# Optimization experiments

Measured on AMD Instinct MI355X. Metric: run time of the kernel, lower is better.

The kernel has to match this reference:

```python
import jax, jax.numpy as jnp
import numpy as np

NEG_SLOPE = 0.2   # PyG GATConv default negative_slope
BN_EPS = 1e-5
N_NODES = 50000
N_EDGES = 600000
N_GRAPHS = 64


def _gat_conv(x, W, att_src, att_dst, bias, src, dst, heads, out_ch, concat):
    """PyG GATConv (eval mode, self-loops already appended to src/dst).
    x: [N, in], W: [in, heads*out_ch], att_*: [heads, out_ch], bias: [heads*out_ch] or [out_ch].
    """
    n = x.shape[0]
    h = (x @ W).reshape(n, heads, out_ch)                  # [N, H, C]
    a_s = jnp.sum(h * att_src[None], axis=-1)              # [N, H]
    a_d = jnp.sum(h * att_dst[None], axis=-1)              # [N, H]
    logit = jax.nn.leaky_relu(a_s[src] + a_d[dst], NEG_SLOPE)  # [E, H]
    # segment softmax over destination node (every node has a self-loop -> no empty segment)
    m = jax.ops.segment_max(logit, dst, num_segments=n)
    p = jnp.exp(logit - m[dst])
    denom = jax.ops.segment_sum(p, dst, num_segments=n)
    alpha = p / (denom[dst] + 1e-16)                       # [E, H]
    out = jax.ops.segment_sum(h[src] * alpha[:, :, None], dst, num_segments=n)  # [N, H, C]
    out = out.reshape(n, heads * out_ch) if concat else out.mean(axis=1)
    return out + bias


def _bn(x, gamma, beta):
    mu = x.mean(axis=0)
    var = x.var(axis=0)
    return (x - mu) * jax.lax.rsqrt(var + BN_EPS) * gamma + beta


def setup_inputs() -> dict:
    key = jax.random.key(0)
    ks = jax.random.split(key, 20)
    hidden = 64
    d1_in, d1_out, h1 = 5, hidden // 2, 4          # 5 -> 32x4 = 128
    d2_in, d2_out, h2 = hidden * 2, hidden // 2, 4  # 128 -> 32x4 = 128
    d3_in, d3_out, h3 = hidden * 2, hidden, 1       # 128 -> 64

    def glorot(k, shape):
        fan = shape[0] + shape[-1]
        return jax.random.normal(k, shape, dtype=jnp.float32) * np.sqrt(2.0 / fan)

    inp = {
        "x": jax.random.normal(ks[0], (N_NODES, d1_in), dtype=jnp.float32),
        "edge_index": jax.random.randint(ks[1], (2, N_EDGES), 0, N_NODES),
        "batch": jnp.sort(jax.random.randint(ks[2], (N_NODES,), 0, N_GRAPHS)),
        # conv1
        "W1": glorot(ks[3], (d1_in, h1 * d1_out)),
        "a1_src": glorot(ks[4], (h1, d1_out)),
        "a1_dst": glorot(ks[5], (h1, d1_out)),
        "b1": jnp.zeros((h1 * d1_out,), dtype=jnp.float32),
        "g1": jnp.ones((h1 * d1_out,), dtype=jnp.float32),
        "be1": jnp.zeros((h1 * d1_out,), dtype=jnp.float32),
        # conv2
        "W2": glorot(ks[6], (d2_in, h2 * d2_out)),
        "a2_src": glorot(ks[7], (h2, d2_out)),
        "a2_dst": glorot(ks[8], (h2, d2_out)),
        "b2": jnp.zeros((h2 * d2_out,), dtype=jnp.float32),
        "g2": jnp.ones((h2 * d2_out,), dtype=jnp.float32),
        "be2": jnp.zeros((h2 * d2_out,), dtype=jnp.float32),
        # conv3 (single head, concat=False)
        "W3": glorot(ks[9], (d3_in, h3 * d3_out)),
        "a3_src": glorot(ks[10], (h3, d3_out)),
        "a3_dst": glorot(ks[11], (h3, d3_out)),
        "b3": jnp.zeros((d3_out,), dtype=jnp.float32),
    }
    return inp


def reference(x, edge_index, batch, W1, a1_src, a1_dst, b1, g1, be1,
              W2, a2_src, a2_dst, b2, g2, be2, W3, a3_src, a3_dst, b3):
    n = x.shape[0]
    loops = jnp.arange(n)
    src = jnp.concatenate([edge_index[0], loops])  # PyG add_self_loops=True
    dst = jnp.concatenate([edge_index[1], loops])

    h = jax.nn.elu(_bn(_gat_conv(x, W1, a1_src, a1_dst, b1, src, dst, 4, 32, True), g1, be1))
    h = jax.nn.elu(_bn(_gat_conv(h, W2, a2_src, a2_dst, b2, src, dst, 4, 32, True), g2, be2))
    h = jax.nn.elu(_gat_conv(h, W3, a3_src, a3_dst, b3, src, dst, 1, 64, False))

    counts = jax.ops.segment_sum(jnp.ones((n,), h.dtype), batch, num_segments=N_GRAPHS)
    mean_pool = jax.ops.segment_sum(h, batch, num_segments=N_GRAPHS) / jnp.maximum(counts, 1.0)[:, None]
    max_pool = jax.ops.segment_max(h, batch, num_segments=N_GRAPHS)
    max_pool = jnp.where(counts[:, None] > 0, max_pool, 0.0)
    return jnp.concatenate([mean_pool, max_pool], axis=1)  # [G, 128]
```

## Files before the change

### kernel.cpp

```cpp
#include <hip/hip_runtime.h>
#include <math.h>

#define NEG_SLOPE 0.2f
#define BN_EPS 1e-5f

typedef __attribute__((ext_vector_type(8))) short short8;
typedef __attribute__((ext_vector_type(4))) float f32x4;

__device__ __forceinline__ float lrelu_f(float x){ return x > 0.f ? x : NEG_SLOPE * x; }
__device__ __forceinline__ float elu_f(float x){ return x > 0.f ? x : __expf(x) - 1.f; }

__device__ __forceinline__ unsigned short f2bf(float f){
    unsigned u = __float_as_uint(f);
    return (unsigned short)((u + 0x7fffu + ((u >> 16) & 1u)) >> 16);
}
__device__ __forceinline__ float bf_lo(unsigned v){ return __uint_as_float(v << 16); }
__device__ __forceinline__ float bf_hi(unsigned v){ return __uint_as_float(v & 0xffff0000u); }
__device__ __forceinline__ float bf2f(unsigned short b){ return __uint_as_float((unsigned)b << 16); }

__device__ __forceinline__ unsigned enc_f(float x){
    unsigned b = __float_as_uint(x);
    return (b & 0x80000000u) ? ~b : (b | 0x80000000u);
}
__device__ __forceinline__ float dec_f(unsigned u){
    return __uint_as_float((u & 0x80000000u) ? (u & 0x7FFFFFFFu) : ~u);
}

__global__ void k_prep(const int* __restrict__ ei, int E0, int N, int Bc, int Bg,
                       const int* __restrict__ batch, int G,
                       int* __restrict__ counts, int* __restrict__ gp,
                       const float* __restrict__ W1, const float* __restrict__ a1s,
                       const float* __restrict__ a1d,
                       const float* __restrict__ W2, const float* __restrict__ W3,
                       unsigned short* __restrict__ wt2, unsigned short* __restrict__ wt3,
                       float* __restrict__ u_s, float* __restrict__ u_d){
    int b = blockIdx.x, tid = threadIdx.x;
    if (b < Bc){
        int i = b * 256 + tid, tot = E0 + N;
        if (i < tot){
            int dst = (i < E0) ? ei[E0 + i] : (i - E0);
            atomicAdd(&counts[dst], 1);
        }
    } else if (b < Bc + Bg){
        int i = (b - Bc) * 256 + tid;
        if (i < N){
            int bb = batch[i];
            if (i == 0){ for (int g = 0; g <= bb; ++g) gp[g] = 0; }
            else { int pb = batch[i - 1]; for (int g = pb + 1; g <= bb; ++g) gp[g] = i; }
            if (i == N - 1){ for (int g = bb + 1; g <= G; ++g) gp[g] = N; }
        }
    } else if (b < Bc + Bg + 96){
        int i = (b - Bc - Bg) * 256 + tid;
        if (i < 128 * 128){
            int k = i / 128, c = i % 128;
            wt2[c * 128 + k] = f2bf(W2[i]);
        } else if (i < 128 * 128 + 128 * 64){
            int j = i - 128 * 128;
            int k = j / 64, c = j % 64;
            wt3[c * 128 + k] = f2bf(W3[j]);
        }
    } else {
        if (tid < 40){
            int t2 = tid % 20;
            int k = t2 / 4, hh = t2 % 4;
            const float* att = (tid < 20) ? a1s : a1d;
            float s = 0.f;
            for (int j = 0; j < 32; ++j) s += W1[k * 128 + hh * 32 + j] * att[hh * 32 + j];
            if (tid < 20) u_s[k * 4 + hh] = s; else u_d[k * 4 + hh] = s;
        }
    }
}

__global__ void k_scan_part(const int* __restrict__ counts, int n, int* __restrict__ part){
    __shared__ int sh[256];
    int tid = threadIdx.x;
    int i = blockIdx.x * 256 + tid;
    int v = (i < n) ? counts[i] : 0;
    sh[tid] = v;
    __syncthreads();
    for (int o = 128; o > 0; o >>= 1){
        if (tid < o) sh[tid] += sh[tid + o];
        __syncthreads();
    }
    if (tid == 0) part[blockIdx.x] = sh[0];
}

__global__ void k_scan_write(const int* __restrict__ counts, const int* __restrict__ part,
                             int n, int* __restrict__ row_ptr){
    __shared__ int sh[256], rsh[256];
    __shared__ int offs;
    int tid = threadIdx.x, bid = blockIdx.x;
    int po = 0;
    for (int j = tid; j < bid; j += 256) po += part[j];
    rsh[tid] = po;
    __syncthreads();
    for (int o = 128; o > 0; o >>= 1){
        if (tid < o) rsh[tid] += rsh[tid + o];
        __syncthreads();
    }
    if (tid == 0) offs = rsh[0];
    __syncthreads();
    int i = bid * 256 + tid;
    int v = (i < n) ? counts[i] : 0;
    sh[tid] = v;
    __syncthreads();
    for (int o = 1; o < 256; o <<= 1){
        int t = (tid >= o) ? sh[tid - o] : 0;
        __syncthreads();
        sh[tid] += t;
        __syncthreads();
    }
    if (i < n) row_ptr[i] = offs + sh[tid] - v;
    if (bid == gridDim.x - 1 && tid == 255) row_ptr[n] = offs + sh[255];
}

__global__ void k_scatter(const int* __restrict__ ei, int E0, int N,
                          const int* __restrict__ row_ptr, int* __restrict__ cursor,
                          int* __restrict__ csr_src){
    int i = blockIdx.x * blockDim.x + threadIdx.x;
    int tot = E0 + N;
    if (i >= tot) return;
    int src, dst;
    if (i < E0){ src = ei[i]; dst = ei[E0 + i]; } else { src = dst = i - E0; }
    int pos = atomicAdd(&cursor[dst], 1);
    csr_src[row_ptr[dst] + pos] = src;
}

__launch_bounds__(256)
__global__ void k_l1(const float* __restrict__ X, const float* __restrict__ W1,
                     const float* __restrict__ u_s, const float* __restrict__ u_d,
                     const int* __restrict__ row_ptr, const int* __restrict__ csr_src,
                     const float* __restrict__ bias, unsigned short* __restrict__ out, int N){
    __shared__ float Wl[5 * 128];
    int tid = threadIdx.x;
    for (int i = tid; i < 5 * 128; i += 256) Wl[i] = W1[i];
    __syncthreads();
    int grp = tid >> 4, ln = tid & 15;
    int hh = ln >> 2, sl = ln & 3;
    long n = (long)blockIdx.x * 16 + grp;
    if (n >= N) return;
    float us[5], ud[5];
#pragma unroll
    for (int k = 0; k < 5; ++k){ us[k] = u_s[k * 4 + hh]; ud[k] = u_d[k * 4 + hh]; }
    float ad = 0.f;
#pragma unroll
    for (int k = 0; k < 5; ++k) ad += X[n * 5 + k] * ud[k];
    int beg = row_ptr[n], end = row_ptr[n + 1];
    float y0 = 0.f, y1 = 0.f, y2 = 0.f, y3 = 0.f, y4 = 0.f, dn = 0.f;
    for (int e = beg + sl; e < end; e += 4){
        long s = csr_src[e];
        float x0 = X[s * 5 + 0], x1 = X[s * 5 + 1], x2 = X[s * 5 + 2],
              x3 = X[s * 5 + 3], x4 = X[s * 5 + 4];
        float as = x0 * us[0] + x1 * us[1] + x2 * us[2] + x3 * us[3] + x4 * us[4];
        float p = __expf(lrelu_f(as + ad));
        dn += p;
        y0 += p * x0; y1 += p * x1; y2 += p * x2; y3 += p * x3; y4 += p * x4;
    }
#pragma unroll
    for (int m = 1; m < 4; m <<= 1){
        y0 += __shfl_xor(y0, m); y1 += __shfl_xor(y1, m); y2 += __shfl_xor(y2, m);
        y3 += __shfl_xor(y3, m); y4 += __shfl_xor(y4, m); dn += __shfl_xor(dn, m);
    }
    float inv = 1.f / dn;
    y0 *= inv; y1 *= inv; y2 *= inv; y3 *= inv; y4 *= inv;
    int c0 = ln * 8;
    const float4* Wl4 = (const float4*)Wl;
    float4 oa, ob;
    {
        float4 w0a = Wl4[0 * 32 + ln * 2], w0b = Wl4[0 * 32 + ln * 2 + 1];
        float4 w1a = Wl4[1 * 32 + ln * 2], w1b = Wl4[1 * 32 + ln * 2 + 1];
        float4 w2a = Wl4[2 * 32 + ln * 2], w2b = Wl4[2 * 32 + ln * 2 + 1];
        float4 w3a = Wl4[3 * 32 + ln * 2], w3b = Wl4[3 * 32 + ln * 2 + 1];
        float4 w4a = Wl4[4 * 32 + ln * 2], w4b = Wl4[4 * 32 + ln * 2 + 1];
        oa.x = y0*w0a.x + y1*w1a.x + y2*w2a.x + y3*w3a.x + y4*w4a.x + bias[c0 + 0];
        oa.y = y0*w0a.y + y1*w1a.y + y2*w2a.y + y3*w3a.y + y4*w4a.y + bias[c0 + 1];
        oa.z = y0*w0a.z + y1*w1a.z + y2*w2a.z + y3*w3a.z + y4*w4a.z + bias[c0 + 2];
        oa.w = y0*w0a.w + y1*w1a.w + y2*w2a.w + y3*w3a.w + y4*w4a.w + bias[c0 + 3];
        ob.x = y0*w0b.x + y1*w1b.x + y2*w2b.x + y3*w3b.x + y4*w4b.x + bias[c0 + 4];
        ob.y = y0*w0b.y + y1*w1b.y + y2*w2b.y + y3*w3b.y + y4*w4b.y + bias[c0 + 5];
        ob.z = y0*w0b.z + y1*w1b.z + y2*w2b.z + y3*w3b.z + y4*w4b.z + bias[c0 + 6];
        ob.w = y0*w0b.w + y1*w1b.w + y2*w2b.w + y3*w3b.w + y4*w4b.w + bias[c0 + 7];
    }
    uint4 o;
    o.x = (unsigned)f2bf(oa.x) | ((unsigned)f2bf(oa.y) << 16);
    o.y = (unsigned)f2bf(oa.z) | ((unsigned)f2bf(oa.w) << 16);
    o.z = (unsigned)f2bf(ob.x) | ((unsigned)f2bf(ob.y) << 16);
    o.w = (unsigned)f2bf(ob.z) | ((unsigned)f2bf(ob.w) << 16);
    *(uint4*)&out[n * 128 + c0] = o;
}

template<int OUT, int H, bool BN>
__launch_bounds__(256)
__global__ void k_gemm_mfma(const unsigned short* __restrict__ X, const unsigned short* __restrict__ Wt,
                            const float* __restrict__ atts, const float* __restrict__ attd,
                            const float* __restrict__ coefs, const float* __restrict__ coefb,
                            unsigned short* __restrict__ h, float* __restrict__ as_,
                            float* __restrict__ ad_, int N){
    constexpr int TM  = 64;
    constexpr int NCT = OUT / 16;
    constexpr int CPH = NCT / H;
    __shared__ unsigned short Xl[TM * 128];
    __shared__ unsigned short Wl[OUT * 128];
    int tid = threadIdx.x;
    long base = (long)blockIdx.x * TM;

    for (int i = tid; i < OUT * 16; i += 256){
        int r = i >> 4, g = i & 15;
        uint4 v = *(const uint4*)&Wt[r * 128 + g * 8];
        int gs = g ^ (r & 7);
        *(uint4*)&Wl[r * 128 + gs * 8] = v;
    }
    for (int i = tid; i < TM * 16; i += 256){
        int r = i >> 4, g = i & 15;
        long node = base + r;
        uint4 o;
        if (node < N){
            uint4 raw = *(const uint4*)&X[node * 128 + g * 8];
            float f[8];
            f[0] = bf_lo(raw.x); f[1] = bf_hi(raw.x);
            f[2] = bf_lo(raw.y); f[3] = bf_hi(raw.y);
            f[4] = bf_lo(raw.z); f[5] = bf_hi(raw.z);
            f[6] = bf_lo(raw.w); f[7] = bf_hi(raw.w);
#pragma unroll
            for (int j = 0; j < 8; ++j){
                float v = f[j];
                if (BN) v = elu_f(fmaf(v, coefs[g * 8 + j], coefb[g * 8 + j]));
                f[j] = v;
            }
            o.x = (unsigned)f2bf(f[0]) | ((unsigned)f2bf(f[1]) << 16);
            o.y = (unsigned)f2bf(f[2]) | ((unsigned)f2bf(f[3]) << 16);
            o.z = (unsigned)f2bf(f[4]) | ((unsigned)f2bf(f[5]) << 16);
            o.w = (unsigned)f2bf(f[6]) | ((unsigned)f2bf(f[7]) << 16);
        } else {
            o.x = o.y = o.z = o.w = 0u;
        }
        int gs = g ^ (r & 7);
        *(uint4*)&Xl[r * 128 + gs * 8] = o;
    }
    __syncthreads();

    int wid = tid >> 6;
    int lane = tid & 63;
    int lr = lane & 15, lk = lane >> 4;

    short8 afrag[4];
    int arow = wid * 16 + lr;
#pragma unroll
    for (int ks = 0; ks < 4; ++ks){
        int g = ks * 4 + lk;
        int gs = g ^ (arow & 7);
        afrag[ks] = *(const short8*)&Xl[arow * 128 + gs * 8];
    }
    f32x4 acc[NCT];
#pragma unroll
    for (int ct = 0; ct < NCT; ++ct) acc[ct] = (f32x4){0.f, 0.f, 0.f, 0.f};
#pragma unroll
    for (int ct = 0; ct < NCT; ++ct){
        int brow = ct * 16 + lr;
#pragma unroll
        for (int ks = 0; ks < 4; ++ks){
            int g = ks * 4 + lk;
            int gs = g ^ (brow & 7);
            short8 bfrag = *(const short8*)&Wl[brow * 128 + gs * 8];
            acc[ct] = __builtin_amdgcn_mfma_f32_16x16x32_bf16(afrag[ks], bfrag, acc[ct], 0, 0, 0);
        }
    }
    float ps[H][4], pd[H][4];
#pragma unroll
    for (int hh = 0; hh < H; ++hh)
#pragma unroll
        for (int j = 0; j < 4; ++j){ ps[hh][j] = 0.f; pd[hh][j] = 0.f; }
#pragma unroll
    for (int ct = 0; ct < NCT; ++ct){
        int col = ct * 16 + lr;
        int hh = ct / CPH;
        float asv = atts[col], adv = attd[col];
#pragma unroll
        for (int j = 0; j < 4; ++j){
            float v = acc[ct][j];
            long node = base + wid * 16 + lk * 4 + j;
            if (node < N) h[node * OUT + col] = f2bf(v);
            ps[hh][j] += v * asv;
            pd[hh][j] += v * adv;
        }
    }
#pragma unroll
    for (int m = 1; m < 16; m <<= 1){
#pragma unroll
        for (int hh = 0; hh < H; ++hh)
#pragma unroll
            for (int j = 0; j < 4; ++j){
                ps[hh][j] += __shfl_xor(ps[hh][j], m);
                pd[hh][j] += __shfl_xor(pd[hh][j], m);
            }
    }
    if (lr == 0){
#pragma unroll
        for (int j = 0; j < 4; ++j){
            long node = base + wid * 16 + lk * 4 + j;
            if (node < N){
#pragma unroll
                for (int hh = 0; hh < H; ++hh){
                    as_[node * H + hh] = ps[hh][j];
                    ad_[node * H + hh] = pd[hh][j];
                }
            }
        }
    }
}

template<int C, int H, int ACT>
__global__ void k_agg(const unsigned short* __restrict__ h, const float* __restrict__ as_,
                      const float* __restrict__ ad_, const int* __restrict__ row_ptr,
                      const int* __restrict__ csr_src, const float* __restrict__ bias,
                      unsigned short* __restrict__ out, int N){
    constexpr int CPL = C / 64;
    constexpr int GROUP = C / H;
    int n = blockIdx.x;
    if (n >= N) return;
    int lane = threadIdx.x;
    int hh = (CPL * lane) / GROUP;
    float ad = ad_[n * H + hh];
    int beg = row_ptr[n], end = row_ptr[n + 1];
    float accx = 0.f, accy = 0.f, dn = 0.f;
    const unsigned* h32 = (const unsigned*)h;
    int e = beg;
    for (; e + 2 <= end; e += 2){
        int s0 = csr_src[e], s1 = csr_src[e + 1];
        float a0 = as_[s0 * H + hh], a1 = as_[s1 * H + hh];
        unsigned v0, v1; unsigned short w0, w1;
        if (CPL == 2){ v0 = h32[(long)s0 * 64 + lane]; v1 = h32[(long)s1 * 64 + lane]; }
        else { w0 = h[(long)s0 * 64 + lane]; w1 = h[(long)s1 * 64 + lane]; }
        float p0 = __expf(lrelu_f(a0 + ad));
        float p1 = __expf(lrelu_f(a1 + ad));
        dn += p0 + p1;
        if (CPL == 2){
            accx += p0 * bf_lo(v0) + p1 * bf_lo(v1);
            accy += p0 * bf_hi(v0) + p1 * bf_hi(v1);
        } else {
            accx += p0 * bf2f(w0) + p1 * bf2f(w1);
        }
    }
    if (e < end){
        int s0 = csr_src[e];
        float p0 = __expf(lrelu_f(as_[s0 * H + hh] + ad));
        dn += p0;
        if (CPL == 2){
            unsigned v0 = h32[(long)s0 * 64 + lane];
            accx += p0 * bf_lo(v0); accy += p0 * bf_hi(v0);
        } else {
            accx += p0 * bf2f(h[(long)s0 * 64 + lane]);
        }
    }
    float inv = 1.f / dn;
    if (CPL == 2){
        float vx = accx * inv + bias[2 * lane];
        float vy = accy * inv + bias[2 * lane + 1];
        if (ACT == 1){ vx = elu_f(vx); vy = elu_f(vy); }
        ((unsigned*)out)[(long)n * 64 + lane] =
            (unsigned)f2bf(vx) | ((unsigned)f2bf(vy) << 16);
    } else {
        float v = accx * inv + bias[lane];
        if (ACT == 1) v = elu_f(v);
        out[(long)n * 64 + lane] = f2bf(v);
    }
}

__launch_bounds__(256)
__global__ void k_bn_part(const unsigned short* __restrict__ x, int N,
                          float* __restrict__ ps, float* __restrict__ pq){
    __shared__ float ls[256 * 8], lq[256 * 8];
    int tid = threadIdx.x;
    int cg = tid & 15;
    int rg = tid >> 4;
    int rpb = (N + gridDim.x - 1) / gridDim.x;
    int lo = blockIdx.x * rpb;
    int hi = lo + rpb; if (hi > N) hi = N;
    float s[8], q[8];
#pragma unroll
    for (int j = 0; j < 8; ++j){ s[j] = 0.f; q[j] = 0.f; }
    int r = lo + rg;
    for (; r + 16 < hi; r += 32){
        uint4 va = *(const uint4*)&x[(long)r * 128 + cg * 8];
        uint4 vb = *(const uint4*)&x[(long)(r + 16) * 128 + cg * 8];
        float fa[8], fb[8];
        fa[0]=bf_lo(va.x); fa[1]=bf_hi(va.x); fa[2]=bf_lo(va.y); fa[3]=bf_hi(va.y);
        fa[4]=bf_lo(va.z); fa[5]=bf_hi(va.z); fa[6]=bf_lo(va.w); fa[7]=bf_hi(va.w);
        fb[0]=bf_lo(vb.x); fb[1]=bf_hi(vb.x); fb[2]=bf_lo(vb.y); fb[3]=bf_hi(vb.y);
        fb[4]=bf_lo(vb.z); fb[5]=bf_hi(vb.z); fb[6]=bf_lo(vb.w); fb[7]=bf_hi(vb.w);
#pragma unroll
        for (int j = 0; j < 8; ++j){
            s[j] += fa[j] + fb[j];
            q[j] += fa[j] * fa[j] + fb[j] * fb[j];
        }
    }
    for (; r < hi; r += 16){
        uint4 va = *(const uint4*)&x[(long)r * 128 + cg * 8];
        float fa[8];
        fa[0]=bf_lo(va.x); fa[1]=bf_hi(va.x); fa[2]=bf_lo(va.y); fa[3]=bf_hi(va.y);
        fa[4]=bf_lo(va.z); fa[5]=bf_hi(va.z); fa[6]=bf_lo(va.w); fa[7]=bf_hi(va.w);
#pragma unroll
        for (int j = 0; j < 8; ++j){ s[j] += fa[j]; q[j] += fa[j] * fa[j]; }
    }
#pragma unroll
    for (int j = 0; j < 8; ++j){ ls[tid * 8 + j] = s[j]; lq[tid * 8 + j] = q[j]; }
    __syncthreads();
    for (int o = 8; o > 0; o >>= 1){
        if (rg < o){
#pragma unroll
            for (int j = 0; j < 8; ++j){
                s[j] += ls[(tid + o * 16) * 8 + j];
                q[j] += lq[(tid + o * 16) * 8 + j];
                ls[tid * 8 + j] = s[j]; lq[tid * 8 + j] = q[j];
            }
        }
        __syncthreads();
    }
    if (rg == 0){
#pragma unroll
        for (int j = 0; j < 8; ++j){
            ps[(long)blockIdx.x * 128 + cg * 8 + j] = s[j];
            pq[(long)blockIdx.x * 128 + cg * 8 + j] = q[j];
        }
    }
}

__launch_bounds__(1024)
__global__ void k_bn_fin(const float* __restrict__ ps, const float* __restrict__ pq, int PB,
                         const float* __restrict__ g, const float* __restrict__ be,
                         float invN, float* __restrict__ cs, float* __restrict__ cb){
    __shared__ float sh_s[1024], sh_q[1024];
    int tid = threadIdx.x;
    int c = tid & 127, sl = tid >> 7;
    float s = 0.f, q = 0.f;
    for (int b = sl; b < PB; b += 8){
        s += ps[(long)b * 128 + c];
        q += pq[(long)b * 128 + c];
    }
    sh_s[tid] = s; sh_q[tid] = q;
    __syncthreads();
    for (int o = 4; o > 0; o >>= 1){
        if (sl < o){
            s += sh_s[tid + o * 128]; q += sh_q[tid + o * 128];
            sh_s[tid] = s; sh_q[tid] = q;
        }
        __syncthreads();
    }
    if (sl == 0){
        float mu = s * invN;
        float var = q * invN - mu * mu;
        float sc = g[c] * rsqrtf(var + BN_EPS);
        cs[c] = sc;
        cb[c] = be[c] - mu * sc;
    }
}

__global__ void k_pool_part(const unsigned short* __restrict__ x, const int* __restrict__ gp,
                            float* __restrict__ psum, unsigned* __restrict__ pmax){
    constexpr int S = 16;
    __shared__ float2 ssum[256], smax[256];
    int g = blockIdx.y;
    int split = blockIdx.x;
    int tid = threadIdx.x;
    int c2 = tid & 31, sub = tid >> 5;
    int beg = gp[g], end = gp[g + 1];
    int len = end - beg;
    int chunk = (len + S - 1) / S;
    int lo = beg + split * chunk;
    int hi = lo + chunk; if (hi > end) hi = end;
    if (lo >= hi) return;
    float sx = 0.f, sy = 0.f, mx = -1e30f, my = -1e30f;
    const unsigned* xr = (const unsigned*)x;
    for (int i = lo + sub; i < hi; i += 8){
        unsigned v = xr[(long)i * 32 + c2];
        float a = bf_lo(v), b = bf_hi(v);
        sx += a; sy += b;
        mx = fmaxf(mx, a); my = fmaxf(my, b);
    }
    ssum[tid] = make_float2(sx, sy); smax[tid] = make_float2(mx, my);
    __syncthreads();
    for (int o = 4; o > 0; o >>= 1){
        if (sub < o){
            float2 s2 = ssum[tid + o * 32], m2 = smax[tid + o * 32];
            sx += s2.x; sy += s2.y;
            mx = fmaxf(mx, m2.x); my = fmaxf(my, m2.y);
            ssum[tid] = make_float2(sx, sy); smax[tid] = make_float2(mx, my);
        }
        __syncthreads();
    }
    if (sub == 0){
        atomicAdd(&psum[g * 64 + c2 * 2], sx);
        atomicAdd(&psum[g * 64 + c2 * 2 + 1], sy);
        atomicMax(&pmax[g * 64 + c2 * 2], enc_f(mx));
        atomicMax(&pmax[g * 64 + c2 * 2 + 1], enc_f(my));
    }
}

__global__ void k_pool_fin(const float* __restrict__ psum, const unsigned* __restrict__ pmax,
                           const int* __restrict__ gp, float* __restrict__ out){
    int g = blockIdx.x;
    int c = threadIdx.x;
    int cnt = gp[g + 1] - gp[g];
    float mean = (cnt > 0) ? psum[g * 64 + c] / (float)cnt : 0.f;
    float mx   = (cnt > 0) ? dec_f(pmax[g * 64 + c]) : 0.f;
    out[g * 128 + c]      = mean;
    out[g * 128 + 64 + c] = mx;
}

extern "C" void kernel_launch(void* const* d_in, const int* in_sizes, int n_in,
                              void* d_out, int out_size, void* d_ws, size_t ws_size,
                              hipStream_t stream){
    const float* x   = (const float*)d_in[0];
    const int*   ei  = (const int*)d_in[1];
    const int*   bat = (const int*)d_in[2];
    const float* W1  = (const float*)d_in[3];
    const float* a1s = (const float*)d_in[4];
    const float* a1d = (const float*)d_in[5];
    const float* b1  = (const float*)d_in[6];
    const float* g1  = (const float*)d_in[7];
    const float* be1 = (const float*)d_in[8];
    const float* W2  = (const float*)d_in[9];
    const float* a2s = (const float*)d_in[10];
    const float* a2d = (const float*)d_in[11];
    const float* b2  = (const float*)d_in[12];
    const float* g2  = (const float*)d_in[13];
    const float* be2 = (const float*)d_in[14];
    const float* W3  = (const float*)d_in[15];
    const float* a3s = (const float*)d_in[16];
    const float* a3d = (const float*)d_in[17];
    const float* b3  = (const float*)d_in[18];
    float* out = (float*)d_out;

    int N  = in_sizes[2];
    int E0 = in_sizes[1] / 2;
    int E  = E0 + N;
    const int G = 64;
    int P  = (N + 255) / 256;
    const int PB = 512;

    char* ws = (char*)d_ws;
    size_t off = 0;
    auto alloc = [&](size_t bytes) -> char* {
        char* p = ws + off;
        off += (bytes + 255) & ~(size_t)255;
        return p;
    };
    int*      counts  = (int*)alloc((size_t)N * 4);
    int*      cursor  = (int*)alloc((size_t)N * 4);
    float*    psum    = (float*)alloc((size_t)G * 64 * 4);
    unsigned* pmax    = (unsigned*)alloc((size_t)G * 64 * 4);
    size_t zero_bytes = off;
    int*   part    = (int*)alloc(256 * 4);
    int*   row_ptr = (int*)alloc((size_t)(N + 1) * 4);
    int*   csr     = (int*)alloc((size_t)E * 4);
    int*   gp      = (int*)alloc((size_t)(G + 1) * 4);
    float* as_buf  = (float*)alloc((size_t)N * 4 * 4);
    float* ad_buf  = (float*)alloc((size_t)N * 4 * 4);
    float* coefs   = (float*)alloc(128 * 4);
    float* coefb   = (float*)alloc(128 * 4);
    float* u_s     = (float*)alloc(20 * 4);
    float* u_d     = (float*)alloc(20 * 4);
    float* bn_ps   = (float*)alloc((size_t)PB * 128 * 4);
    float* bn_pq   = (float*)alloc((size_t)PB * 128 * 4);
    unsigned short* wt2 = (unsigned short*)alloc(128 * 128 * 2);
    unsigned short* wt3 = (unsigned short*)alloc(64 * 128 * 2);
    unsigned short* hbuf = (unsigned short*)alloc((size_t)N * 128 * 2);
    unsigned short* xcur = (unsigned short*)alloc((size_t)N * 128 * 2);

    hipMemsetAsync(ws, 0, zero_bytes, stream);

    int Bc = (E + 255) / 256, Bg = (N + 255) / 256;
    k_prep<<<Bc + Bg + 96 + 1, 256, 0, stream>>>(ei, E0, N, Bc, Bg, bat, G, counts, gp,
                                                 W1, a1s, a1d, W2, W3, wt2, wt3, u_s, u_d);
    k_scan_part<<<P, 256, 0, stream>>>(counts, N, part);
    k_scan_write<<<P, 256, 0, stream>>>(counts, part, N, row_ptr);
    k_scatter<<<(E + 255) / 256, 256, 0, stream>>>(ei, E0, N, row_ptr, cursor, csr);

    k_l1<<<(N + 15) / 16, 256, 0, stream>>>(x, W1, u_s, u_d, row_ptr, csr, b1, xcur, N);
    k_bn_part<<<PB, 256, 0, stream>>>(xcur, N, bn_ps, bn_pq);
    k_bn_fin<<<1, 1024, 0, stream>>>(bn_ps, bn_pq, PB, g1, be1, 1.f / N, coefs, coefb);

    k_gemm_mfma<128, 4, true><<<(N + 63) / 64, 256, 0, stream>>>(
        xcur, wt2, a2s, a2d, coefs, coefb, hbuf, as_buf, ad_buf, N);
    k_agg<128, 4, 0><<<N, 64, 0, stream>>>(hbuf, as_buf, ad_buf, row_ptr, csr, b2, xcur, N);
    k_bn_part<<<PB, 256, 0, stream>>>(xcur, N, bn_ps, bn_pq);
    k_bn_fin<<<1, 1024, 0, stream>>>(bn_ps, bn_pq, PB, g2, be2, 1.f / N, coefs, coefb);

    k_gemm_mfma<64, 1, true><<<(N + 63) / 64, 256, 0, stream>>>(
        xcur, wt3, a3s, a3d, coefs, coefb, hbuf, as_buf, ad_buf, N);
    k_agg<64, 1, 1><<<N, 64, 0, stream>>>(hbuf, as_buf, ad_buf, row_ptr, csr, b3, xcur, N);

    {
        dim3 grid(16, G);
        k_pool_part<<<grid, 256, 0, stream>>>(xcur, gp, psum, pmax);
        k_pool_fin<<<G, 64, 0, stream>>>(psum, pmax, gp, out);
    }
}
```

Before: 233.1 us.

## Fuse BN statistics and pooling into aggregation kernels, merge scan kernels

Layer-1 and layer-2 aggregation kernels now compute per-block batch-norm partial sums. Layer 2 accumulates them into 256 atomic buckets, which removes the separate k_bn_part passes over the activations. The layer-3 aggregation does mean and max pooling directly with segment-leader atomics, so the final activation write and the k_pool_part pass go away. The two-pass scan becomes one kernel that re-sums counts directly, and aggregation now packs 8 nodes per 512-thread block with 4-way unrolled edge loops. The cost is more atomics and a quadratic prefix re-read in the scan.

After: 353.4 us. 1.52x slower.

```diff
diff --git a/kernel.cpp b/kernel.cpp
--- a/kernel.cpp
+++ b/kernel.cpp
@@ -71,27 +71,13 @@
     }
 }
 
-__global__ void k_scan_part(const int* __restrict__ counts, int n, int* __restrict__ part){
-    __shared__ int sh[256];
-    int tid = threadIdx.x;
-    int i = blockIdx.x * 256 + tid;
-    int v = (i < n) ? counts[i] : 0;
-    sh[tid] = v;
-    __syncthreads();
-    for (int o = 128; o > 0; o >>= 1){
-        if (tid < o) sh[tid] += sh[tid + o];
-        __syncthreads();
-    }
-    if (tid == 0) part[blockIdx.x] = sh[0];
-}
-
-__global__ void k_scan_write(const int* __restrict__ counts, const int* __restrict__ part,
-                             int n, int* __restrict__ row_ptr){
+__global__ void k_scan(const int* __restrict__ counts, int n, int* __restrict__ row_ptr){
     __shared__ int sh[256], rsh[256];
     __shared__ int offs;
     int tid = threadIdx.x, bid = blockIdx.x;
+    int limit = bid * 256;
     int po = 0;
-    for (int j = tid; j < bid; j += 256) po += part[j];
+    for (int j = tid; j < limit; j += 256) po += counts[j];
     rsh[tid] = po;
     __syncthreads();
     for (int o = 128; o > 0; o >>= 1){
@@ -100,7 +86,7 @@
     }
     if (tid == 0) offs = rsh[0];
     __syncthreads();
-    int i = bid * 256 + tid;
+    int i = limit + tid;
     int v = (i < n) ? counts[i] : 0;
     sh[tid] = v;
     __syncthreads();
@@ -130,22 +116,27 @@
 __global__ void k_l1(const float* __restrict__ X, const float* __restrict__ W1,
                      const float* __restrict__ u_s, const float* __restrict__ u_d,
                      const int* __restrict__ row_ptr, const int* __restrict__ csr_src,
-                     const float* __restrict__ bias, unsigned short* __restrict__ out, int N){
+                     const float* __restrict__ bias, unsigned short* __restrict__ out,
+                     float* __restrict__ bn_ps, float* __restrict__ bn_pq, int N){
     __shared__ float Wl[5 * 128];
+    __shared__ float bs[16][128], bq[16][128];
     int tid = threadIdx.x;
     for (int i = tid; i < 5 * 128; i += 256) Wl[i] = W1[i];
     __syncthreads();
     int grp = tid >> 4, ln = tid & 15;
     int hh = ln >> 2, sl = ln & 3;
     long n = (long)blockIdx.x * 16 + grp;
-    if (n >= N) return;
+    bool valid = n < N;
     float us[5], ud[5];
 #pragma unroll
     for (int k = 0; k < 5; ++k){ us[k] = u_s[k * 4 + hh]; ud[k] = u_d[k * 4 + hh]; }
     float ad = 0.f;
-#pragma unroll
-    for (int k = 0; k < 5; ++k) ad += X[n * 5 + k] * ud[k];
-    int beg = row_ptr[n], end = row_ptr[n + 1];
+    if (valid){
+#pragma unroll
+        for (int k = 0; k < 5; ++k) ad += X[n * 5 + k] * ud[k];
+    }
+    int beg = 0, end = 0;
+    if (valid){ beg = row_ptr[n]; end = row_ptr[n + 1]; }
     float y0 = 0.f, y1 = 0.f, y2 = 0.f, y3 = 0.f, y4 = 0.f, dn = 0.f;
     for (int e = beg + sl; e < end; e += 4){
         long s = csr_src[e];
@@ -161,12 +152,12 @@
         y0 += __shfl_xor(y0, m); y1 += __shfl_xor(y1, m); y2 += __shfl_xor(y2, m);
         y3 += __shfl_xor(y3, m); y4 += __shfl_xor(y4, m); dn += __shfl_xor(dn, m);
     }
-    float inv = 1.f / dn;
+    float inv = valid ? 1.f / dn : 0.f;
     y0 *= inv; y1 *= inv; y2 *= inv; y3 *= inv; y4 *= inv;
     int c0 = ln * 8;
     const float4* Wl4 = (const float4*)Wl;
-    float4 oa, ob;
-    {
+    float4 oa = {0,0,0,0}, ob = {0,0,0,0};
+    if (valid){
         float4 w0a = Wl4[0 * 32 + ln * 2], w0b = Wl4[0 * 32 + ln * 2 + 1];
         float4 w1a = Wl4[1 * 32 + ln * 2], w1b = Wl4[1 * 32 + ln * 2 + 1];
         float4 w2a = Wl4[2 * 32 + ln * 2], w2b = Wl4[2 * 32 + ln * 2 + 1];
@@ -180,13 +171,34 @@
         ob.y = y0*w0b.y + y1*w1b.y + y2*w2b.y + y3*w3b.y + y4*w4b.y + bias[c0 + 5];
         ob.z = y0*w0b.z + y1*w1b.z + y2*w2b.z + y3*w3b.z + y4*w4b.z + bias[c0 + 6];
         ob.w = y0*w0b.w + y1*w1b.w + y2*w2b.w + y3*w3b.w + y4*w4b.w + bias[c0 + 7];
-    }
-    uint4 o;
-    o.x = (unsigned)f2bf(oa.x) | ((unsigned)f2bf(oa.y) << 16);
-    o.y = (unsigned)f2bf(oa.z) | ((unsigned)f2bf(oa.w) << 16);
-    o.z = (unsigned)f2bf(ob.x) | ((unsigned)f2bf(ob.y) << 16);
-    o.w = (unsigned)f2bf(ob.z) | ((unsigned)f2bf(ob.w) << 16);
-    *(uint4*)&out[n * 128 + c0] = o;
+        uint4 o;
+        o.x = (unsigned)f2bf(oa.x) | ((unsigned)f2bf(oa.y) << 16);
+        o.y = (unsigned)f2bf(oa.z) | ((unsigned)f2bf(oa.w) << 16);
+        o.z = (unsigned)f2bf(ob.x) | ((unsigned)f2bf(ob.y) << 16);
+        o.w = (unsigned)f2bf(ob.z) | ((unsigned)f2bf(ob.w) << 16);
+        *(uint4*)&out[n * 128 + c0] = o;
+    }
+    float ov[8] = {oa.x, oa.y, oa.z, oa.w, ob.x, ob.y, ob.z, ob.w};
+#pragma unroll
+    for (int j = 0; j < 8; ++j){ bs[grp][c0 + j] = ov[j]; bq[grp][c0 + j] = ov[j] * ov[j]; }
+    __syncthreads();
+    for (int o = 8; o > 0; o >>= 1){
+        if (grp < o){
+#pragma unroll
+            for (int j = 0; j < 8; ++j){
+                bs[grp][c0 + j] += bs[grp + o][c0 + j];
+                bq[grp][c0 + j] += bq[grp + o][c0 + j];
+            }
+        }
+        __syncthreads();
+    }
+    if (grp == 0){
+#pragma unroll
+        for (int j = 0; j < 8; ++j){
+            bn_ps[(long)blockIdx.x * 128 + c0 + j] = bs[0][c0 + j];
+            bn_pq[(long)blockIdx.x * 128 + c0 + j] = bq[0][c0 + j];
+        }
+    }
 }
 
 template<int OUT, int H, bool BN>
@@ -309,119 +321,122 @@
     }
 }
 
-template<int C, int H, int ACT>
-__global__ void k_agg(const unsigned short* __restrict__ h, const float* __restrict__ as_,
-                      const float* __restrict__ ad_, const int* __restrict__ row_ptr,
-                      const int* __restrict__ csr_src, const float* __restrict__ bias,
-                      unsigned short* __restrict__ out, int N){
-    constexpr int CPL = C / 64;
-    constexpr int GROUP = C / H;
-    int n = blockIdx.x;
-    if (n >= N) return;
-    int lane = threadIdx.x;
-    int hh = (CPL * lane) / GROUP;
-    float ad = ad_[n * H + hh];
-    int beg = row_ptr[n], end = row_ptr[n + 1];
-    float accx = 0.f, accy = 0.f, dn = 0.f;
-    const unsigned* h32 = (const unsigned*)h;
-    int e = beg;
-    for (; e + 2 <= end; e += 2){
-        int s0 = csr_src[e], s1 = csr_src[e + 1];
-        float a0 = as_[s0 * H + hh], a1 = as_[s1 * H + hh];
-        unsigned v0, v1; unsigned short w0, w1;
-        if (CPL == 2){ v0 = h32[(long)s0 * 64 + lane]; v1 = h32[(long)s1 * 64 + lane]; }
-        else { w0 = h[(long)s0 * 64 + lane]; w1 = h[(long)s1 * 64 + lane]; }
-        float p0 = __expf(lrelu_f(a0 + ad));
-        float p1 = __expf(lrelu_f(a1 + ad));
-        dn += p0 + p1;
-        if (CPL == 2){
-            accx += p0 * bf_lo(v0) + p1 * bf_lo(v1);
-            accy += p0 * bf_hi(v0) + p1 * bf_hi(v1);
-        } else {
-            accx += p0 * bf2f(w0) + p1 * bf2f(w1);
-        }
-    }
-    if (e < end){
-        int s0 = csr_src[e];
-        float p0 = __expf(lrelu_f(as_[s0 * H + hh] + ad));
-        dn += p0;
-        if (CPL == 2){
-            unsigned v0 = h32[(long)s0 * 64 + lane];
+__launch_bounds__(512)
+__global__ void k_agg2(const unsigned short* __restrict__ h, const float* __restrict__ as_,
+                       const float* __restrict__ ad_, const int* __restrict__ row_ptr,
+                       const int* __restrict__ csr_src, const float* __restrict__ bias,
+                       unsigned short* __restrict__ out,
+                       float* __restrict__ bnb_s, float* __restrict__ bnb_q, int N){
+    __shared__ float ls[8][128], lq[8][128];
+    int tid = threadIdx.x;
+    int wid = tid >> 6, lane = tid & 63;
+    long n = (long)blockIdx.x * 8 + wid;
+    bool valid = n < N;
+    int hh = lane >> 4;
+    float vx = 0.f, vy = 0.f;
+    if (valid){
+        float ad = ad_[n * 4 + hh];
+        int beg = row_ptr[n], end = row_ptr[n + 1];
+        float accx = 0.f, accy = 0.f, dn = 0.f;
+        const unsigned* h32 = (const unsigned*)h;
+        int e = beg;
+        for (; e + 4 <= end; e += 4){
+            int s0 = csr_src[e], s1 = csr_src[e+1], s2 = csr_src[e+2], s3 = csr_src[e+3];
+            float a0 = as_[s0*4+hh], a1 = as_[s1*4+hh], a2 = as_[s2*4+hh], a3 = as_[s3*4+hh];
+            unsigned v0 = h32[(long)s0*64+lane], v1 = h32[(long)s1*64+lane],
+                     v2 = h32[(long)s2*64+lane], v3 = h32[(long)s3*64+lane];
+            float p0 = __expf(lrelu_f(a0 + ad));
+            float p1 = __expf(lrelu_f(a1 + ad));
+            float p2 = __expf(lrelu_f(a2 + ad));
+            float p3 = __expf(lrelu_f(a3 + ad));
+            dn += p0 + p1 + p2 + p3;
+            accx += p0*bf_lo(v0) + p1*bf_lo(v1) + p2*bf_lo(v2) + p3*bf_lo(v3);
+            accy += p0*bf_hi(v0) + p1*bf_hi(v1) + p2*bf_hi(v2) + p3*bf_hi(v3);
+        }
+        for (; e < end; ++e){
+            int s0 = csr_src[e];
+            unsigned v0 = h32[(long)s0*64+lane];
+            float p0 = __expf(lrelu_f(as_[s0*4+hh] + ad));
+            dn += p0;
             accx += p0 * bf_lo(v0); accy += p0 * bf_hi(v0);
-        } else {
-            accx += p0 * bf2f(h[(long)s0 * 64 + lane]);
-        }
-    }
-    float inv = 1.f / dn;
-    if (CPL == 2){
-        float vx = accx * inv + bias[2 * lane];
-        float vy = accy * inv + bias[2 * lane + 1];
-        if (ACT == 1){ vx = elu_f(vx); vy = elu_f(vy); }
-        ((unsigned*)out)[(long)n * 64 + lane] =
-            (unsigned)f2bf(vx) | ((unsigned)f2bf(vy) << 16);
-    } else {
-        float v = accx * inv + bias[lane];
-        if (ACT == 1) v = elu_f(v);
-        out[(long)n * 64 + lane] = f2bf(v);
-    }
-}
-
-__launch_bounds__(256)
-__global__ void k_bn_part(const unsigned short* __restrict__ x, int N,
-                          float* __restrict__ ps, float* __restrict__ pq){
-    __shared__ float ls[256 * 8], lq[256 * 8];
+        }
+        float inv = 1.f / dn;
+        vx = accx * inv + bias[2*lane];
+        vy = accy * inv + bias[2*lane + 1];
+        ((unsigned*)out)[n * 64 + lane] = (unsigned)f2bf(vx) | ((unsigned)f2bf(vy) << 16);
+    }
+    ls[wid][2*lane] = vx; ls[wid][2*lane+1] = vy;
+    lq[wid][2*lane] = vx*vx; lq[wid][2*lane+1] = vy*vy;
+    __syncthreads();
+    for (int o = 4; o > 0; o >>= 1){
+        if (wid < o){
+            ls[wid][2*lane]   += ls[wid+o][2*lane];
+            ls[wid][2*lane+1] += ls[wid+o][2*lane+1];
+            lq[wid][2*lane]   += lq[wid+o][2*lane];
+            lq[wid][2*lane+1] += lq[wid+o][2*lane+1];
+        }
+        __syncthreads();
+    }
+    if (wid == 0){
+        int bucket = blockIdx.x & 255;
+        atomicAdd(&bnb_s[bucket*128 + 2*lane],   ls[0][2*lane]);
+        atomicAdd(&bnb_s[bucket*128 + 2*lane+1], ls[0][2*lane+1]);
+        atomicAdd(&bnb_q[bucket*128 + 2*lane],   lq[0][2*lane]);
+        atomicAdd(&bnb_q[bucket*128 + 2*lane+1], lq[0][2*lane+1]);
+    }
+}
+
+__launch_bounds__(512)
+__global__ void k_agg3(const unsigned short* __restrict__ h, const float* __restrict__ as_,
+                       const float* __restrict__ ad_, const int* __restrict__ row_ptr,
+                       const int* __restrict__ csr_src, const float* __restrict__ bias,
+                       const int* __restrict__ batch,
+                       float* __restrict__ psum, unsigned* __restrict__ pmax, int N){
+    __shared__ float lsv[8][64];
+    __shared__ int lg[8];
     int tid = threadIdx.x;
-    int cg = tid & 15;
-    int rg = tid >> 4;
-    int rpb = (N + gridDim.x - 1) / gridDim.x;
-    int lo = blockIdx.x * rpb;
-    int hi = lo + rpb; if (hi > N) hi = N;
-    float s[8], q[8];
-#pragma unroll
-    for (int j = 0; j < 8; ++j){ s[j] = 0.f; q[j] = 0.f; }
-    int r = lo + rg;
-    for (; r + 16 < hi; r += 32){
-        uint4 va = *(const uint4*)&x[(long)r * 128 + cg * 8];
-        uint4 vb = *(const uint4*)&x[(long)(r + 16) * 128 + cg * 8];
-        float fa[8], fb[8];
-        fa[0]=bf_lo(va.x); fa[1]=bf_hi(va.x); fa[2]=bf_lo(va.y); fa[3]=bf_hi(va.y);
-        fa[4]=bf_lo(va.z); fa[5]=bf_hi(va.z); fa[6]=bf_lo(va.w); fa[7]=bf_hi(va.w);
-        fb[0]=bf_lo(vb.x); fb[1]=bf_hi(vb.x); fb[2]=bf_lo(vb.y); fb[3]=bf_hi(vb.y);
-        fb[4]=bf_lo(vb.z); fb[5]=bf_hi(vb.z); fb[6]=bf_lo(vb.w); fb[7]=bf_hi(vb.w);
-#pragma unroll
-        for (int j = 0; j < 8; ++j){
-            s[j] += fa[j] + fb[j];
-            q[j] += fa[j] * fa[j] + fb[j] * fb[j];
-        }
-    }
-    for (; r < hi; r += 16){
-        uint4 va = *(const uint4*)&x[(long)r * 128 + cg * 8];
-        float fa[8];
-        fa[0]=bf_lo(va.x); fa[1]=bf_hi(va.x); fa[2]=bf_lo(va.y); fa[3]=bf_hi(va.y);
-        fa[4]=bf_lo(va.z); fa[5]=bf_hi(va.z); fa[6]=bf_lo(va.w); fa[7]=bf_hi(va.w);
-#pragma unroll
-        for (int j = 0; j < 8; ++j){ s[j] += fa[j]; q[j] += fa[j] * fa[j]; }
-    }
-#pragma unroll
-    for (int j = 0; j < 8; ++j){ ls[tid * 8 + j] = s[j]; lq[tid * 8 + j] = q[j]; }
-    __syncthreads();
-    for (int o = 8; o > 0; o >>= 1){
-        if (rg < o){
-#pragma unroll
-            for (int j = 0; j < 8; ++j){
-                s[j] += ls[(tid + o * 16) * 8 + j];
-                q[j] += lq[(tid + o * 16) * 8 + j];
-                ls[tid * 8 + j] = s[j]; lq[tid * 8 + j] = q[j];
-            }
-        }
-        __syncthreads();
-    }
-    if (rg == 0){
-#pragma unroll
-        for (int j = 0; j < 8; ++j){
-            ps[(long)blockIdx.x * 128 + cg * 8 + j] = s[j];
-            pq[(long)blockIdx.x * 128 + cg * 8 + j] = q[j];
-        }
+    int wid = tid >> 6, lane = tid & 63;
+    long n = (long)blockIdx.x * 8 + wid;
+    bool valid = n < N;
+    float v = 0.f;
+    if (valid){
+        float ad = ad_[n];
+        int beg = row_ptr[n], end = row_ptr[n + 1];
+        float acc = 0.f, dn = 0.f;
+        int e = beg;
+        for (; e + 4 <= end; e += 4){
+            int s0 = csr_src[e], s1 = csr_src[e+1], s2 = csr_src[e+2], s3 = csr_src[e+3];
+            float a0 = as_[s0], a1 = as_[s1], a2 = as_[s2], a3 = as_[s3];
+            unsigned short w0 = h[(long)s0*64+lane], w1 = h[(long)s1*64+lane],
+                           w2 = h[(long)s2*64+lane], w3 = h[(long)s3*64+lane];
+            float p0 = __expf(lrelu_f(a0 + ad));
+            float p1 = __expf(lrelu_f(a1 + ad));
+            float p2 = __expf(lrelu_f(a2 + ad));
+            float p3 = __expf(lrelu_f(a3 + ad));
+            dn += p0 + p1 + p2 + p3;
+            acc += p0*bf2f(w0) + p1*bf2f(w1) + p2*bf2f(w2) + p3*bf2f(w3);
+        }
+        for (; e < end; ++e){
+            int s0 = csr_src[e];
+            float p0 = __expf(lrelu_f(as_[s0] + ad));
+            dn += p0;
+            acc += p0 * bf2f(h[(long)s0*64+lane]);
+        }
+        v = elu_f(acc / dn + bias[lane]);
+    }
+    if (lane == 0) lg[wid] = valid ? batch[n] : -1;
+    lsv[wid][lane] = v;
+    __syncthreads();
+    int gw = lg[wid];
+    bool leader = (gw >= 0) && (wid == 0 || lg[wid - 1] != gw);
+    if (leader){
+        float s = 0.f, m = -1e30f;
+        for (int w = wid; w < 8 && lg[w] == gw; ++w){
+            float x = lsv[w][lane];
+            s += x; m = fmaxf(m, x);
+        }
+        atomicAdd(&psum[gw * 64 + lane], s);
+        atomicMax(&pmax[gw * 64 + lane], enc_f(m));
     }
 }
 
@@ -452,47 +467,6 @@
         float sc = g[c] * rsqrtf(var + BN_EPS);
         cs[c] = sc;
         cb[c] = be[c] - mu * sc;
-    }
-}
-
-__global__ void k_pool_part(const unsigned short* __restrict__ x, const int* __restrict__ gp,
-                            float* __restrict__ psum, unsigned* __restrict__ pmax){
-    constexpr int S = 16;
-    __shared__ float2 ssum[256], smax[256];
-    int g = blockIdx.y;
-    int split = blockIdx.x;
-    int tid = threadIdx.x;
-    int c2 = tid & 31, sub = tid >> 5;
-    int beg = gp[g], end = gp[g + 1];
-    int len = end - beg;
-    int chunk = (len + S - 1) / S;
-    int lo = beg + split * chunk;
-    int hi = lo + chunk; if (hi > end) hi = end;
-    if (lo >= hi) return;
-    float sx = 0.f, sy = 0.f, mx = -1e30f, my = -1e30f;
-    const unsigned* xr = (const unsigned*)x;
-    for (int i = lo + sub; i < hi; i += 8){
-        unsigned v = xr[(long)i * 32 + c2];
-        float a = bf_lo(v), b = bf_hi(v);
-        sx += a; sy += b;
-        mx = fmaxf(mx, a); my = fmaxf(my, b);
-    }
-    ssum[tid] = make_float2(sx, sy); smax[tid] = make_float2(mx, my);
-    __syncthreads();
-    for (int o = 4; o > 0; o >>= 1){
-        if (sub < o){
-            float2 s2 = ssum[tid + o * 32], m2 = smax[tid + o * 32];
-            sx += s2.x; sy += s2.y;
-            mx = fmaxf(mx, m2.x); my = fmaxf(my, m2.y);
-            ssum[tid] = make_float2(sx, sy); smax[tid] = make_float2(mx, my);
-        }
-        __syncthreads();
-    }
-    if (sub == 0){
-        atomicAdd(&psum[g * 64 + c2 * 2], sx);
-        atomicAdd(&psum[g * 64 + c2 * 2 + 1], sy);
-        atomicMax(&pmax[g * 64 + c2 * 2], enc_f(mx));
-        atomicMax(&pmax[g * 64 + c2 * 2 + 1], enc_f(my));
     }
 }
 
@@ -536,7 +510,8 @@
     int E  = E0 + N;
     const int G = 64;
     int P  = (N + 255) / 256;
-    const int PB = 512;
+    int PB1 = (N + 15) / 16;
+    const int NB = 256;
 
     char* ws = (char*)d_ws;
     size_t off = 0;
@@ -549,8 +524,9 @@
     int*      cursor  = (int*)alloc((size_t)N * 4);
     float*    psum    = (float*)alloc((size_t)G * 64 * 4);
     unsigned* pmax    = (unsigned*)alloc((size_t)G * 64 * 4);
+    float*    bnb_s   = (float*)alloc((size_t)NB * 128 * 4);
+    float*    bnb_q   = (float*)alloc((size_t)NB * 128 * 4);
     size_t zero_bytes = off;
-    int*   part    = (int*)alloc(256 * 4);
     int*   row_ptr = (int*)alloc((size_t)(N + 1) * 4);
     int*   csr     = (int*)alloc((size_t)E * 4);
     int*   gp      = (int*)alloc((size_t)(G + 1) * 4);
@@ -560,8 +536,8 @@
     float* coefb   = (float*)alloc(128 * 4);
     float* u_s     = (float*)alloc(20 * 4);
     float* u_d     = (float*)alloc(20 * 4);
-    float* bn_ps   = (float*)alloc((size_t)PB * 128 * 4);
-    float* bn_pq   = (float*)alloc((size_t)PB * 128 * 4);
+    float* bn_ps   = (float*)alloc((size_t)PB1 * 128 * 4);
+    float* bn_pq   = (float*)alloc((size_t)PB1 * 128 * 4);
     unsigned short* wt2 = (unsigned short*)alloc(128 * 128 * 2);
     unsigned short* wt3 = (unsigned short*)alloc(64 * 128 * 2);
     unsigned short* hbuf = (unsigned short*)alloc((size_t)N * 128 * 2);
@@ -572,27 +548,21 @@
     int Bc = (E + 255) / 256, Bg = (N + 255) / 256;
     k_prep<<<Bc + Bg + 96 + 1, 256, 0, stream>>>(ei, E0, N, Bc, Bg, bat, G, counts, gp,
                                                  W1, a1s, a1d, W2, W3, wt2, wt3, u_s, u_d);
-    k_scan_part<<<P, 256, 0, stream>>>(counts, N, part);
-    k_scan_write<<<P, 256, 0, stream>>>(counts, part, N, row_ptr);
+    k_scan<<<P, 256, 0, stream>>>(counts, N, row_ptr);
     k_scatter<<<(E + 255) / 256, 256, 0, stream>>>(ei, E0, N, row_ptr, cursor, csr);
 
-    k_l1<<<(N + 15) / 16, 256, 0, stream>>>(x, W1, u_s, u_d, row_ptr, csr, b1, xcur, N);
-    k_bn_part<<<PB, 256, 0, stream>>>(xcur, N, bn_ps, bn_pq);
-    k_bn_fin<<<1, 1024, 0, stream>>>(bn_ps, bn_pq, PB, g1, be1, 1.f / N, coefs, coefb);
+    k_l1<<<PB1, 256, 0, stream>>>(x, W1, u_s, u_d, row_ptr, csr, b1, xcur, bn_ps, bn_pq, N);
+    k_bn_fin<<<1, 1024, 0, stream>>>(bn_ps, bn_pq, PB1, g1, be1, 1.f / N, coefs, coefb);
 
     k_gemm_mfma<128, 4, true><<<(N + 63) / 64, 256, 0, stream>>>(
         xcur, wt2, a2s, a2d, coefs, coefb, hbuf, as_buf, ad_buf, N);
-    k_agg<128, 4, 0><<<N, 64, 0, stream>>>(hbuf, as_buf, ad_buf, row_ptr, csr, b2, xcur, N);
-    k_bn_part<<<PB, 256, 0, stream>>>(xcur, N, bn_ps, bn_pq);
-    k_bn_fin<<<1, 1024, 0, stream>>>(bn_ps, bn_pq, PB, g2, be2, 1.f / N, coefs, coefb);
+    k_agg2<<<(N + 7) / 8, 512, 0, stream>>>(hbuf, as_buf, ad_buf, row_ptr, csr, b2,
+                                            xcur, bnb_s, bnb_q, N);
+    k_bn_fin<<<1, 1024, 0, stream>>>(bnb_s, bnb_q, NB, g2, be2, 1.f / N, coefs, coefb);
 
     k_gemm_mfma<64, 1, true><<<(N + 63) / 64, 256, 0, stream>>>(
         xcur, wt3, a3s, a3d, coefs, coefb, hbuf, as_buf, ad_buf, N);
-    k_agg<64, 1, 1><<<N, 64, 0, stream>>>(hbuf, as_buf, ad_buf, row_ptr, csr, b3, xcur, N);
-
-    {
-        dim3 grid(16, G);
-        k_pool_part<<<grid, 256, 0, stream>>>(xcur, gp, psum, pmax);
-        k_pool_fin<<<G, 64, 0, stream>>>(psum, pmax, gp, out);
-    }
-}
+    k_agg3<<<(N + 7) / 8, 512, 0, stream>>>(hbuf, as_buf, ad_buf, row_ptr, csr, b3,
+                                            bat, psum, pmax, N);
+    k_pool_fin<<<G, 64, 0, stream>>>(psum, pmax, gp, out);
+}
```
